# Kernel optimization log

Measured on AMD Instinct MI355X. Metric: run time of the kernel, lower is better.

The kernel has to match this reference:

```python
import jax, jax.numpy as jnp
import numpy as np

N = 50000      # nodes
E = 800000     # edges (before self loops)
D = 256        # in_features
SMALL = 25     # floor(D/10)


def setup_inputs() -> dict:
    key = jax.random.key(0)
    k1, k2, k3, k4, k5 = jax.random.split(key, 5)
    x = jax.random.normal(k1, (N, D), jnp.float32)
    src = jax.random.randint(k2, (E,), 0, N)
    dst = jax.random.randint(k3, (E,), 0, N)
    Wq = jax.random.normal(k4, (D, SMALL), jnp.float32) / np.float32(np.sqrt(D))
    bq = jnp.zeros((SMALL,), jnp.float32)
    Wk = jax.random.normal(k5, (D, SMALL), jnp.float32) / np.float32(np.sqrt(D))
    bk = jnp.zeros((SMALL,), jnp.float32)
    return {"x": x, "src": src, "dst": dst, "Wq": Wq, "bq": bq, "Wk": Wk, "bk": bk}


def reference(x, src, dst, Wq, bq, Wk, bk):
    d_k = np.float32(np.sqrt(SMALL))  # self.d_k = sqrt(small_in_features)
    q = jnp.tanh(x @ Wq + bq)         # query head: Linear + Tanh, [N, SMALL]
    k = x @ Wk + bk                   # key head: Linear,          [N, SMALL]
    # dgl.add_self_loop: append (i, i) for every node
    loop = jnp.arange(N, dtype=src.dtype)
    s = jnp.concatenate([src, loop])  # [E+N]
    d = jnp.concatenate([dst, loop])  # [E+N]
    # edge weight = <query[src], key[dst]> / d_k
    w = jnp.sum(q[s] * k[d], axis=1) / d_k            # [E+N]
    # segment softmax over incoming edges of each destination node
    wmax = jax.ops.segment_max(w, d, num_segments=N)  # every node has a self loop -> no empty segments
    ew = jnp.exp(w - wmax[d])
    denom = jax.ops.segment_sum(ew, d, num_segments=N)
    alpha = ew / denom[d]                             # [E+N]
    # weighted scatter-sum of src node features
    out = jax.ops.segment_sum(alpha[:, None] * x[s], d, num_segments=N)  # [N, D]
    return out
```

## Files before the change

### kernel.cpp

```cpp
#include <hip/hip_runtime.h>
#include <math.h>

#define D 256
#define SM 25
#define QS 32
#define WROWS 264
#define NCH 4

typedef short bf16x8 __attribute__((ext_vector_type(8)));
typedef float f32x4  __attribute__((ext_vector_type(4)));

__device__ __forceinline__ unsigned int bf16rne(float f) {
    unsigned int u = __float_as_uint(f);
    return (u + 0x7fffu + ((u >> 16) & 1u)) >> 16;
}
__device__ __forceinline__ float bl(unsigned int lo16) {
    return __uint_as_float(lo16 << 16);
}
__device__ __forceinline__ float bh(unsigned int u) {
    return __uint_as_float(u & 0xffff0000u);
}

__global__ __launch_bounds__(256) void prep_kernel(
    const float* __restrict__ Wq, const float* __restrict__ bq,
    const float* __restrict__ Wk, const float* __restrict__ bk,
    unsigned short* __restrict__ wt_g,
    float* __restrict__ bias_g,
    int* __restrict__ cnt, int N) {
    int gid = blockIdx.x * 256 + threadIdx.x;
    if (gid < N) cnt[gid] = 0;
    if (gid < 64 * 256) {
        int j = gid >> 8, k = gid & 255;
        float w = 0.f;
        if (j < SM) w = Wq[k * SM + j];
        else if (j < 2 * SM) w = Wk[k * SM + (j - SM)];
        wt_g[j * 256 + k] = (unsigned short)bf16rne(w);
    }
    if (gid >= 16384 && gid < 16448) {
        int t = gid - 16384;
        bias_g[t] = (t < SM) ? bq[t] : ((t < 2 * SM) ? bk[t - SM] : 0.f);
    }
}

__global__ __launch_bounds__(256) void qk_kernel(
    const float* __restrict__ x,
    const unsigned short* __restrict__ wt_g, const float* __restrict__ bias_g,
    const int4* __restrict__ dst4, const int* __restrict__ dste,
    unsigned short* __restrict__ xh,
    float* __restrict__ qp,
    float* __restrict__ kp,
    int* __restrict__ cnt, int N, int E) {
    __shared__ __align__(16) short xs[64 * WROWS];
    __shared__ __align__(16) short wt[64 * WROWS];
    __shared__ float bias[64];
    int t = threadIdx.x;
    int n0 = blockIdx.x * 64;

    {
        int r = t >> 2, qtr = t & 3;
        int row = n0 + r; if (row >= N) row = N - 1;
        const float4* xr = (const float4*)(x + (size_t)row * D) + qtr * 16;
        short* dst = xs + r * WROWS + qtr * 64;
#pragma unroll
        for (int i = 0; i < 16; ++i) {
            float4 a = xr[i];
            unsigned int w0 = bf16rne(a.x) | (bf16rne(a.y) << 16);
            unsigned int w1 = bf16rne(a.z) | (bf16rne(a.w) << 16);
            *(uint2*)(dst + i * 4) = make_uint2(w0, w1);
        }
    }
#pragma unroll
    for (int o = 0; o < 8; ++o) {
        int idx = o * 256 + t;
        int j = idx >> 5, k8 = idx & 31;
        *(uint4*)(wt + j * WROWS + k8 * 8) = ((const uint4*)wt_g)[idx];
    }
    if (t < 64) bias[t] = bias_g[t];
    __syncthreads();

    for (int o = 0; o < 8; ++o) {
        int idx = o * 256 + t;
        int r = idx >> 5, c = idx & 31;
        int row = n0 + r;
        if (row < N) {
            uint4 v = *(const uint4*)(xs + r * WROWS + c * 8);
            *((uint4*)(xh + (size_t)row * D) + c) = v;
        }
    }

    int wid = t >> 6, lane = t & 63;
    int mm = lane & 15, g = lane >> 4;
    f32x4 acc[4];
#pragma unroll
    for (int tt = 0; tt < 4; ++tt) acc[tt] = (f32x4){0.f, 0.f, 0.f, 0.f};
    const short* arow = xs + (wid * 16 + mm) * WROWS + g * 8;
#pragma unroll
    for (int ks = 0; ks < 8; ++ks) {
        bf16x8 af = *(const bf16x8*)(arow + ks * 32);
#pragma unroll
        for (int tt = 0; tt < 4; ++tt) {
            bf16x8 bf = *(const bf16x8*)(wt + (tt * 16 + mm) * WROWS + g * 8 + ks * 32);
            acc[tt] = __builtin_amdgcn_mfma_f32_16x16x32_bf16(af, bf, acc[tt], 0, 0, 0);
        }
    }
#pragma unroll
    for (int tt = 0; tt < 4; ++tt) {
        int j = tt * 16 + mm;
#pragma unroll
        for (int r = 0; r < 4; ++r) {
            int node = n0 + wid * 16 + g * 4 + r;
            if (node >= N) continue;
            float v = acc[tt][r] + bias[j];
            if (j < SM)           qp[(size_t)node * QS + j] = tanhf(v);
            else if (j < 2 * SM)  kp[(size_t)node * QS + (j - SM)] = v;
            else if (j < 57)      qp[(size_t)node * QS + (j - SM)] = 0.f;
            else                  kp[(size_t)node * QS + (j - 32)] = 0.f;
        }
    }

    int gid = blockIdx.x * 256 + t;
    int n4e = E >> 2;
    if (gid < n4e) {
        int4 dd = dst4[gid];
        atomicAdd(&cnt[dd.x], 1);
        atomicAdd(&cnt[dd.y], 1);
        atomicAdd(&cnt[dd.z], 1);
        atomicAdd(&cnt[dd.w], 1);
    }
    if (gid == 0) {
        for (int e = n4e * 4; e < E; ++e) atomicAdd(&cnt[dste[e]], 1);
    }
}

__global__ __launch_bounds__(256) void scan_a_kernel(const int4* __restrict__ cnt4,
                                                     int* __restrict__ bsum, int n4) {
    __shared__ int wsum[4];
    int t = threadIdx.x;
    int idx = blockIdx.x * 256 + t;
    int s = 0;
    if (idx < n4) { int4 v = cnt4[idx]; s = v.x + v.y + v.z + v.w; }
#pragma unroll
    for (int o = 32; o; o >>= 1) s += __shfl_xor(s, o);
    if ((t & 63) == 0) wsum[t >> 6] = s;
    __syncthreads();
    if (t == 0) bsum[blockIdx.x] = wsum[0] + wsum[1] + wsum[2] + wsum[3];
}

__global__ __launch_bounds__(256) void scan_c_kernel(const int4* __restrict__ cnt4,
                                                     const int* __restrict__ bsum,
                                                     int* __restrict__ offN,
                                                     int4* __restrict__ off4,
                                                     int4* __restrict__ cursor4,
                                                     int n4, int nblk) {
    __shared__ int wsum[4];
    int t = threadIdx.x;
    int lane = t & 63;
    int bv = (lane < nblk) ? bsum[lane] : 0;
    int bincl = bv;
#pragma unroll
    for (int o = 1; o < 64; o <<= 1) {
        int u = __shfl_up(bincl, o);
        if (lane >= o) bincl += u;
    }
    int blockbase = __shfl(bincl - bv, blockIdx.x);
    int total = __shfl(bincl, nblk - 1);
    if (blockIdx.x == 0 && t == 0) *offN = total;
    int idx = blockIdx.x * 256 + t;
    int4 v = make_int4(0, 0, 0, 0);
    if (idx < n4) v = cnt4[idx];
    int s0 = v.x, s01 = s0 + v.y, s012 = s01 + v.z, s = s012 + v.w;
    int incl = s;
#pragma unroll
    for (int o = 1; o < 64; o <<= 1) {
        int u = __shfl_up(incl, o);
        if (lane >= o) incl += u;
    }
    if (lane == 63) wsum[t >> 6] = incl;
    __syncthreads();
    int w = t >> 6;
    int wbase = 0;
    for (int i = 0; i < w; ++i) wbase += wsum[i];
    int base = blockbase + wbase + (incl - s);
    if (idx < n4) {
        int4 o4 = make_int4(base, base + s0, base + s01, base + s012);
        off4[idx]    = o4;
        cursor4[idx] = o4;
    }
}

__global__ void scatter_kernel(const int4* __restrict__ src4, const int4* __restrict__ dst4,
                               const int* __restrict__ srce, const int* __restrict__ dste,
                               int* __restrict__ cursor, int* __restrict__ csr_src,
                               int n4e, int E) {
    int e = blockIdx.x * blockDim.x + threadIdx.x;
    if (e >= n4e) return;
    int4 s = src4[e];
    int4 d = dst4[e];
    csr_src[atomicAdd(&cursor[d.x], 1)] = s.x;
    csr_src[atomicAdd(&cursor[d.y], 1)] = s.y;
    csr_src[atomicAdd(&cursor[d.z], 1)] = s.z;
    csr_src[atomicAdd(&cursor[d.w], 1)] = s.w;
    if (e == 0) {
        for (int i = n4e * 4; i < E; ++i)
            csr_src[atomicAdd(&cursor[dste[i]], 1)] = srce[i];
    }
}

__global__ __launch_bounds__(256) void agg_kernel(
        const uint2* __restrict__ xh2, const float* __restrict__ qp,
        const float* __restrict__ kp, const int* __restrict__ off,
        const int* __restrict__ csr_src, float4* __restrict__ out4, int N) {
    int lane = threadIdx.x & 63;
    int v = blockIdx.x * 4 + (threadIdx.x >> 6);
    if (v >= N) return;
    int lo = off[v];
    int deg1 = off[v + 1] - lo + 1;
    const float4* kd4 = (const float4*)(kp + (size_t)v * QS);
    float4 kd[7];
#pragma unroll
    for (int j = 0; j < 7; ++j) kd[j] = kd4[j];

    float wv[NCH]; int sv[NCH];
    float m = -INFINITY;
#pragma unroll
    for (int c = 0; c < NCH; ++c) {
        int i = c * 64 + lane;
        float wcur = -INFINITY; int s = v;
        if (c * 64 < deg1 && i < deg1) {
            if (i > 0) s = csr_src[lo + i - 1];
            const float4* q4 = (const float4*)(qp + (size_t)s * QS);
            float acc = 0.f;
#pragma unroll
            for (int j = 0; j < 7; ++j) {
                float4 a = q4[j];
                acc += a.x*kd[j].x + a.y*kd[j].y + a.z*kd[j].z + a.w*kd[j].w;
            }
            wcur = acc * 0.2f;
        }
        wv[c] = wcur; sv[c] = s;
        m = fmaxf(m, wcur);
    }
#pragma unroll
    for (int o = 32; o; o >>= 1) m = fmaxf(m, __shfl_xor(m, o));
    float ssum = 0.f;
#pragma unroll
    for (int c = 0; c < NCH; ++c) {
        float e = (wv[c] == -INFINITY) ? 0.f : __expf(wv[c] - m);
        wv[c] = e;
        ssum += e;
    }
#pragma unroll
    for (int o = 32; o; o >>= 1) ssum += __shfl_xor(ssum, o);
    float inv = 1.f / ssum;

    const uint2* xb = xh2 + lane;
    float4 acc = make_float4(0.f, 0.f, 0.f, 0.f);
#pragma unroll
    for (int c = 0; c < NCH; ++c) {
        if (c * 64 >= deg1) break;
        int cnt = deg1 - c * 64; if (cnt > 64) cnt = 64;
        int j = 0;
        for (; j + 8 <= cnt; j += 8) {
            float a0 = __shfl(wv[c], j);     int s0 = __shfl(sv[c], j);
            float a1 = __shfl(wv[c], j + 1); int s1 = __shfl(sv[c], j + 1);
            float a2 = __shfl(wv[c], j + 2); int s2 = __shfl(sv[c], j + 2);
            float a3 = __shfl(wv[c], j + 3); int s3 = __shfl(sv[c], j + 3);
            float a4 = __shfl(wv[c], j + 4); int s4 = __shfl(sv[c], j + 4);
            float a5 = __shfl(wv[c], j + 5); int s5 = __shfl(sv[c], j + 5);
            float a6 = __shfl(wv[c], j + 6); int s6 = __shfl(sv[c], j + 6);
            float a7 = __shfl(wv[c], j + 7); int s7 = __shfl(sv[c], j + 7);
            uint2 u0 = xb[(size_t)s0 * 64];
            uint2 u1 = xb[(size_t)s1 * 64];
            uint2 u2 = xb[(size_t)s2 * 64];
            uint2 u3 = xb[(size_t)s3 * 64];
            uint2 u4 = xb[(size_t)s4 * 64];
            uint2 u5 = xb[(size_t)s5 * 64];
            uint2 u6 = xb[(size_t)s6 * 64];
            uint2 u7 = xb[(size_t)s7 * 64];
            acc.x += a0 * bl(u0.x); acc.y += a0 * bh(u0.x);
            acc.z += a0 * bl(u0.y); acc.w += a0 * bh(u0.y);
            acc.x += a1 * bl(u1.x); acc.y += a1 * bh(u1.x);
            acc.z += a1 * bl(u1.y); acc.w += a1 * bh(u1.y);
            acc.x += a2 * bl(u2.x); acc.y += a2 * bh(u2.x);
            acc.z += a2 * bl(u2.y); acc.w += a2 * bh(u2.y);
            acc.x += a3 * bl(u3.x); acc.y += a3 * bh(u3.x);
            acc.z += a3 * bl(u3.y); acc.w += a3 * bh(u3.y);
            acc.x += a4 * bl(u4.x); acc.y += a4 * bh(u4.x);
            acc.z += a4 * bl(u4.y); acc.w += a4 * bh(u4.y);
            acc.x += a5 * bl(u5.x); acc.y += a5 * bh(u5.x);
            acc.z += a5 * bl(u5.y); acc.w += a5 * bh(u5.y);
            acc.x += a6 * bl(u6.x); acc.y += a6 * bh(u6.x);
            acc.z += a6 * bl(u6.y); acc.w += a6 * bh(u6.y);
            acc.x += a7 * bl(u7.x); acc.y += a7 * bh(u7.x);
            acc.z += a7 * bl(u7.y); acc.w += a7 * bh(u7.y);
        }
        for (; j + 4 <= cnt; j += 4) {
            float a0 = __shfl(wv[c], j);     int s0 = __shfl(sv[c], j);
            float a1 = __shfl(wv[c], j + 1); int s1 = __shfl(sv[c], j + 1);
            float a2 = __shfl(wv[c], j + 2); int s2 = __shfl(sv[c], j + 2);
            float a3 = __shfl(wv[c], j + 3); int s3 = __shfl(sv[c], j + 3);
            uint2 u0 = xb[(size_t)s0 * 64];
            uint2 u1 = xb[(size_t)s1 * 64];
            uint2 u2 = xb[(size_t)s2 * 64];
            uint2 u3 = xb[(size_t)s3 * 64];
            acc.x += a0 * bl(u0.x); acc.y += a0 * bh(u0.x);
            acc.z += a0 * bl(u0.y); acc.w += a0 * bh(u0.y);
            acc.x += a1 * bl(u1.x); acc.y += a1 * bh(u1.x);
            acc.z += a1 * bl(u1.y); acc.w += a1 * bh(u1.y);
            acc.x += a2 * bl(u2.x); acc.y += a2 * bh(u2.x);
            acc.z += a2 * bl(u2.y); acc.w += a2 * bh(u2.y);
            acc.x += a3 * bl(u3.x); acc.y += a3 * bh(u3.x);
            acc.z += a3 * bl(u3.y); acc.w += a3 * bh(u3.y);
        }
        for (; j < cnt; ++j) {
            float a = __shfl(wv[c], j);
            int   s = __shfl(sv[c], j);
            uint2 u = xb[(size_t)s * 64];
            acc.x += a * bl(u.x); acc.y += a * bh(u.x);
            acc.z += a * bl(u.y); acc.w += a * bh(u.y);
        }
    }
    acc.x *= inv; acc.y *= inv; acc.z *= inv; acc.w *= inv;
    out4[(size_t)v * 64 + lane] = acc;
}

extern "C" void kernel_launch(void* const* d_in, const int* in_sizes, int n_in,
                              void* d_out, int out_size, void* d_ws, size_t ws_size,
                              hipStream_t stream) {
    const float* x   = (const float*)d_in[0];
    const int*   src = (const int*)d_in[1];
    const int*   dst = (const int*)d_in[2];
    const float* Wq  = (const float*)d_in[3];
    const float* bq  = (const float*)d_in[4];
    const float* Wk  = (const float*)d_in[5];
    const float* bk  = (const float*)d_in[6];
    float* out = (float*)d_out;

    int N = in_sizes[0] / D;
    int E = in_sizes[1];

    char* p = (char*)d_ws;
    auto alloc = [&](size_t bytes) {
        char* r = p;
        p += (bytes + 255) & ~(size_t)255;
        return r;
    };
    unsigned short* xh   = (unsigned short*)alloc((size_t)N * D * sizeof(unsigned short));
    unsigned short* wt_g = (unsigned short*)alloc(64 * 256 * sizeof(unsigned short));
    float* bias_g  = (float*)alloc(64 * sizeof(float));
    float* qp      = (float*)alloc((size_t)N * QS * sizeof(float));
    float* kp      = (float*)alloc((size_t)N * QS * sizeof(float));
    int*   cnt     = (int*)  alloc((size_t)(N + 4) * sizeof(int));
    int*   off     = (int*)  alloc((size_t)(N + 4) * sizeof(int));
    int*   cursor  = (int*)  alloc((size_t)(N + 4) * sizeof(int));
    int*   csr_src = (int*)  alloc((size_t)E * sizeof(int));
    int*   bsum    = (int*)  alloc(64 * sizeof(int));

    int prepgrid = (N > 16448 ? N : 16448);
    prep_kernel<<<(prepgrid + 255) / 256, 256, 0, stream>>>(
        Wq, bq, Wk, bk, wt_g, bias_g, cnt, N);
    int nqk = (N + 63) / 64;
    qk_kernel<<<nqk, 256, 0, stream>>>(x, wt_g, bias_g, (const int4*)dst, dst,
                                       xh, qp, kp, cnt, N, E);
    int n4 = (N + 3) / 4;
    int nblk = (n4 + 255) / 256;
    scan_a_kernel<<<nblk, 256, 0, stream>>>((const int4*)cnt, bsum, n4);
    scan_c_kernel<<<nblk, 256, 0, stream>>>((const int4*)cnt, bsum, off + N,
                                            (int4*)off, (int4*)cursor, n4, nblk);
    int n4e = E / 4;
    scatter_kernel<<<(n4e + 255) / 256, 256, 0, stream>>>(
        (const int4*)src, (const int4*)dst, src, dst, cursor, csr_src, n4e, E);
    agg_kernel<<<(N + 3) / 4, 256, 0, stream>>>(
        (const uint2*)xh, qp, kp, off, csr_src, (float4*)out, N);
}
```

Baseline: 278.2 us.

## Split aggregation into score and feature-tiled gather kernels with tiled bf16 layout

The fused aggregation kernel is split in two. A score kernel computes softmax-normalized edge weights and writes them to global arrays, and a gather kernel processes the 256 features in 8 tiles of 32. The bf16 copy of x is stored tile-major so each tile's gather working set is smaller and more cache-friendly. The qk kernel also reads the weight matrix directly from global memory instead of staging it in shared memory. This adds a kernel launch, extra traffic for the alpha arrays, and repeated CSR/alpha reads across the 8 tiles, in exchange for better L2 locality on the random row gathers.

```diff
diff --git a/kernel.cpp b/kernel.cpp
--- a/kernel.cpp
+++ b/kernel.cpp
@@ -6,6 +6,7 @@
 #define QS 32
 #define WROWS 264
 #define NCH 4
+#define NT 8
 
 typedef short bf16x8 __attribute__((ext_vector_type(8)));
 typedef float f32x4  __attribute__((ext_vector_type(4)));
@@ -46,12 +47,11 @@
     const float* __restrict__ x,
     const unsigned short* __restrict__ wt_g, const float* __restrict__ bias_g,
     const int4* __restrict__ dst4, const int* __restrict__ dste,
-    unsigned short* __restrict__ xh,
+    unsigned short* __restrict__ xt,
     float* __restrict__ qp,
     float* __restrict__ kp,
     int* __restrict__ cnt, int N, int E) {
     __shared__ __align__(16) short xs[64 * WROWS];
-    __shared__ __align__(16) short wt[64 * WROWS];
     __shared__ float bias[64];
     int t = threadIdx.x;
     int n0 = blockIdx.x * 64;
@@ -68,12 +68,6 @@
             unsigned int w1 = bf16rne(a.z) | (bf16rne(a.w) << 16);
             *(uint2*)(dst + i * 4) = make_uint2(w0, w1);
         }
-    }
-#pragma unroll
-    for (int o = 0; o < 8; ++o) {
-        int idx = o * 256 + t;
-        int j = idx >> 5, k8 = idx & 31;
-        *(uint4*)(wt + j * WROWS + k8 * 8) = ((const uint4*)wt_g)[idx];
     }
     if (t < 64) bias[t] = bias_g[t];
     __syncthreads();
@@ -84,7 +78,8 @@
         int row = n0 + r;
         if (row < N) {
             uint4 v = *(const uint4*)(xs + r * WROWS + c * 8);
-            *((uint4*)(xh + (size_t)row * D) + c) = v;
+            int tile = c >> 2;
+            ((uint4*)xt)[((size_t)tile * N + row) * 4 + (c & 3)] = v;
         }
     }
 
@@ -99,7 +94,8 @@
         bf16x8 af = *(const bf16x8*)(arow + ks * 32);
 #pragma unroll
         for (int tt = 0; tt < 4; ++tt) {
-            bf16x8 bf = *(const bf16x8*)(wt + (tt * 16 + mm) * WROWS + g * 8 + ks * 32);
+            bf16x8 bf = *(const bf16x8*)((const short*)wt_g +
+                                         (tt * 16 + mm) * 256 + g * 8 + ks * 32);
             acc[tt] = __builtin_amdgcn_mfma_f32_16x16x32_bf16(af, bf, acc[tt], 0, 0, 0);
         }
     }
@@ -206,10 +202,10 @@
     }
 }
 
-__global__ __launch_bounds__(256) void agg_kernel(
-        const uint2* __restrict__ xh2, const float* __restrict__ qp,
-        const float* __restrict__ kp, const int* __restrict__ off,
-        const int* __restrict__ csr_src, float4* __restrict__ out4, int N) {
+__global__ __launch_bounds__(256) void score_kernel(
+        const float* __restrict__ qp, const float* __restrict__ kp,
+        const int* __restrict__ off, const int* __restrict__ csr_src,
+        float* __restrict__ alphaS, float* __restrict__ alphaE, int N) {
     int lane = threadIdx.x & 63;
     int v = blockIdx.x * 4 + (threadIdx.x >> 6);
     if (v >= N) return;
@@ -220,13 +216,14 @@
 #pragma unroll
     for (int j = 0; j < 7; ++j) kd[j] = kd4[j];
 
-    float wv[NCH]; int sv[NCH];
+    float wv[NCH];
     float m = -INFINITY;
 #pragma unroll
     for (int c = 0; c < NCH; ++c) {
         int i = c * 64 + lane;
-        float wcur = -INFINITY; int s = v;
+        float wcur = -INFINITY;
         if (c * 64 < deg1 && i < deg1) {
+            int s = v;
             if (i > 0) s = csr_src[lo + i - 1];
             const float4* q4 = (const float4*)(qp + (size_t)s * QS);
             float acc = 0.f;
@@ -237,7 +234,7 @@
             }
             wcur = acc * 0.2f;
         }
-        wv[c] = wcur; sv[c] = s;
+        wv[c] = wcur;
         m = fmaxf(m, wcur);
     }
 #pragma unroll
@@ -253,75 +250,59 @@
     for (int o = 32; o; o >>= 1) ssum += __shfl_xor(ssum, o);
     float inv = 1.f / ssum;
 
-    const uint2* xb = xh2 + lane;
-    float4 acc = make_float4(0.f, 0.f, 0.f, 0.f);
 #pragma unroll
     for (int c = 0; c < NCH; ++c) {
-        if (c * 64 >= deg1) break;
-        int cnt = deg1 - c * 64; if (cnt > 64) cnt = 64;
-        int j = 0;
-        for (; j + 8 <= cnt; j += 8) {
-            float a0 = __shfl(wv[c], j);     int s0 = __shfl(sv[c], j);
-            float a1 = __shfl(wv[c], j + 1); int s1 = __shfl(sv[c], j + 1);
-            float a2 = __shfl(wv[c], j + 2); int s2 = __shfl(sv[c], j + 2);
-            float a3 = __shfl(wv[c], j + 3); int s3 = __shfl(sv[c], j + 3);
-            float a4 = __shfl(wv[c], j + 4); int s4 = __shfl(sv[c], j + 4);
-            float a5 = __shfl(wv[c], j + 5); int s5 = __shfl(sv[c], j + 5);
-            float a6 = __shfl(wv[c], j + 6); int s6 = __shfl(sv[c], j + 6);
-            float a7 = __shfl(wv[c], j + 7); int s7 = __shfl(sv[c], j + 7);
-            uint2 u0 = xb[(size_t)s0 * 64];
-            uint2 u1 = xb[(size_t)s1 * 64];
-            uint2 u2 = xb[(size_t)s2 * 64];
-            uint2 u3 = xb[(size_t)s3 * 64];
-            uint2 u4 = xb[(size_t)s4 * 64];
-            uint2 u5 = xb[(size_t)s5 * 64];
-            uint2 u6 = xb[(size_t)s6 * 64];
-            uint2 u7 = xb[(size_t)s7 * 64];
-            acc.x += a0 * bl(u0.x); acc.y += a0 * bh(u0.x);
-            acc.z += a0 * bl(u0.y); acc.w += a0 * bh(u0.y);
-            acc.x += a1 * bl(u1.x); acc.y += a1 * bh(u1.x);
-            acc.z += a1 * bl(u1.y); acc.w += a1 * bh(u1.y);
-            acc.x += a2 * bl(u2.x); acc.y += a2 * bh(u2.x);
-            acc.z += a2 * bl(u2.y); acc.w += a2 * bh(u2.y);
-            acc.x += a3 * bl(u3.x); acc.y += a3 * bh(u3.x);
-            acc.z += a3 * bl(u3.y); acc.w += a3 * bh(u3.y);
-            acc.x += a4 * bl(u4.x); acc.y += a4 * bh(u4.x);
-            acc.z += a4 * bl(u4.y); acc.w += a4 * bh(u4.y);
-            acc.x += a5 * bl(u5.x); acc.y += a5 * bh(u5.x);
-            acc.z += a5 * bl(u5.y); acc.w += a5 * bh(u5.y);
-            acc.x += a6 * bl(u6.x); acc.y += a6 * bh(u6.x);
-            acc.z += a6 * bl(u6.y); acc.w += a6 * bh(u6.y);
-            acc.x += a7 * bl(u7.x); acc.y += a7 * bh(u7.x);
-            acc.z += a7 * bl(u7.y); acc.w += a7 * bh(u7.y);
-        }
-        for (; j + 4 <= cnt; j += 4) {
-            float a0 = __shfl(wv[c], j);     int s0 = __shfl(sv[c], j);
-            float a1 = __shfl(wv[c], j + 1); int s1 = __shfl(sv[c], j + 1);
-            float a2 = __shfl(wv[c], j + 2); int s2 = __shfl(sv[c], j + 2);
-            float a3 = __shfl(wv[c], j + 3); int s3 = __shfl(sv[c], j + 3);
-            uint2 u0 = xb[(size_t)s0 * 64];
-            uint2 u1 = xb[(size_t)s1 * 64];
-            uint2 u2 = xb[(size_t)s2 * 64];
-            uint2 u3 = xb[(size_t)s3 * 64];
-            acc.x += a0 * bl(u0.x); acc.y += a0 * bh(u0.x);
-            acc.z += a0 * bl(u0.y); acc.w += a0 * bh(u0.y);
-            acc.x += a1 * bl(u1.x); acc.y += a1 * bh(u1.x);
-            acc.z += a1 * bl(u1.y); acc.w += a1 * bh(u1.y);
-            acc.x += a2 * bl(u2.x); acc.y += a2 * bh(u2.x);
-            acc.z += a2 * bl(u2.y); acc.w += a2 * bh(u2.y);
-            acc.x += a3 * bl(u3.x); acc.y += a3 * bh(u3.x);
-            acc.z += a3 * bl(u3.y); acc.w += a3 * bh(u3.y);
-        }
-        for (; j < cnt; ++j) {
-            float a = __shfl(wv[c], j);
-            int   s = __shfl(sv[c], j);
-            uint2 u = xb[(size_t)s * 64];
-            acc.x += a * bl(u.x); acc.y += a * bh(u.x);
-            acc.z += a * bl(u.y); acc.w += a * bh(u.y);
-        }
-    }
-    acc.x *= inv; acc.y *= inv; acc.z *= inv; acc.w *= inv;
-    out4[(size_t)v * 64 + lane] = acc;
+        int i = c * 64 + lane;
+        if (c * 64 < deg1 && i < deg1) {
+            float a = wv[c] * inv;
+            if (i == 0) alphaS[v] = a;
+            else        alphaE[lo + i - 1] = a;
+        }
+    }
+}
+
+__global__ __launch_bounds__(256) void gather_kernel(
+        const unsigned int* __restrict__ xt,
+        const float* __restrict__ alphaS, const float* __restrict__ alphaE,
+        const int* __restrict__ off, const int* __restrict__ csr_src,
+        float* __restrict__ out, int N) {
+    int tile = blockIdx.x & (NT - 1);
+    int nb = blockIdx.x >> 3;
+    int t = threadIdx.x;
+    int g = t >> 4;
+    int l = t & 15;
+    int v = nb * 16 + g;
+    if (v >= N) return;
+    const unsigned int* xbase = xt + (size_t)tile * N * 16 + l;
+    int lo = off[v], hi = off[v + 1];
+    float ax = 0.f, ay = 0.f;
+    {
+        float a = alphaS[v];
+        unsigned int u = xbase[(size_t)v * 16];
+        ax += a * bl(u); ay += a * bh(u);
+    }
+    int e = lo;
+    for (; e + 4 <= hi; e += 4) {
+        float a0 = alphaE[e];     int s0 = csr_src[e];
+        float a1 = alphaE[e + 1]; int s1 = csr_src[e + 1];
+        float a2 = alphaE[e + 2]; int s2 = csr_src[e + 2];
+        float a3 = alphaE[e + 3]; int s3 = csr_src[e + 3];
+        unsigned int u0 = xbase[(size_t)s0 * 16];
+        unsigned int u1 = xbase[(size_t)s1 * 16];
+        unsigned int u2 = xbase[(size_t)s2 * 16];
+        unsigned int u3 = xbase[(size_t)s3 * 16];
+        ax += a0 * bl(u0); ay += a0 * bh(u0);
+        ax += a1 * bl(u1); ay += a1 * bh(u1);
+        ax += a2 * bl(u2); ay += a2 * bh(u2);
+        ax += a3 * bl(u3); ay += a3 * bh(u3);
+    }
+    for (; e < hi; ++e) {
+        float a = alphaE[e];
+        int   s = csr_src[e];
+        unsigned int u = xbase[(size_t)s * 16];
+        ax += a * bl(u); ay += a * bh(u);
+    }
+    *(float2*)(out + (size_t)v * D + tile * 32 + l * 2) = make_float2(ax, ay);
 }
 
 extern "C" void kernel_launch(void* const* d_in, const int* in_sizes, int n_in,
@@ -345,7 +326,7 @@
         p += (bytes + 255) & ~(size_t)255;
         return r;
     };
-    unsigned short* xh   = (unsigned short*)alloc((size_t)N * D * sizeof(unsigned short));
+    unsigned short* xt   = (unsigned short*)alloc((size_t)N * D * sizeof(unsigned short));
     unsigned short* wt_g = (unsigned short*)alloc(64 * 256 * sizeof(unsigned short));
     float* bias_g  = (float*)alloc(64 * sizeof(float));
     float* qp      = (float*)alloc((size_t)N * QS * sizeof(float));
@@ -355,13 +336,15 @@
     int*   cursor  = (int*)  alloc((size_t)(N + 4) * sizeof(int));
     int*   csr_src = (int*)  alloc((size_t)E * sizeof(int));
     int*   bsum    = (int*)  alloc(64 * sizeof(int));
+    float* alphaS  = (float*)alloc((size_t)N * sizeof(float));
+    float* alphaE  = (float*)alloc((size_t)E * sizeof(float));
 
     int prepgrid = (N > 16448 ? N : 16448);
     prep_kernel<<<(prepgrid + 255) / 256, 256, 0, stream>>>(
         Wq, bq, Wk, bk, wt_g, bias_g, cnt, N);
     int nqk = (N + 63) / 64;
     qk_kernel<<<nqk, 256, 0, stream>>>(x, wt_g, bias_g, (const int4*)dst, dst,
-                                       xh, qp, kp, cnt, N, E);
+                                       xt, qp, kp, cnt, N, E);
     int n4 = (N + 3) / 4;
     int nblk = (n4 + 255) / 256;
     scan_a_kernel<<<nblk, 256, 0, stream>>>((const int4*)cnt, bsum, n4);
@@ -370,6 +353,10 @@
     int n4e = E / 4;
     scatter_kernel<<<(n4e + 255) / 256, 256, 0, stream>>>(
         (const int4*)src, (const int4*)dst, src, dst, cursor, csr_src, n4e, E);
-    agg_kernel<<<(N + 3) / 4, 256, 0, stream>>>(
-        (const uint2*)xh, qp, kp, off, csr_src, (float4*)out, N);
-}
+    score_kernel<<<(N + 3) / 4, 256, 0, stream>>>(qp, kp, off, csr_src,
+                                                  alphaS, alphaE, N);
+    int ngb = (N + 15) / 16;
+    gather_kernel<<<ngb * NT, 256, 0, stream>>>((const unsigned int*)xt,
+                                                alphaS, alphaE, off, csr_src,
+                                                out, N);
+}
```

Result: slower. 325.8 us (+17.1%).

## Split edge dot products across four lanes and read QK weights from global

Applied to the files above, without the earlier changes.

In the aggregation kernel, each edge's 25-wide query·key dot product is now split across four lanes, each doing 8 elements, and combined with xor-shuffles. A wave therefore scores 16 edges per chunk instead of 64, which cuts per-lane serial loads and the number of lanes left idle on low-degree nodes. The trade-off is capacity: with NCHK=4 a node can now hold at most 64 incoming edges, down from 256. The projection kernel also drops the LDS staging of the weight matrix and loads B fragments straight from global/L2, saving LDS and one copy phase at the cost of repeated global reads.

```diff
diff --git a/kernel.cpp b/kernel.cpp
--- a/kernel.cpp
+++ b/kernel.cpp
@@ -5,7 +5,7 @@
 #define SM 25
 #define QS 32
 #define WROWS 264
-#define NCH 4
+#define NCHK 4
 
 typedef short bf16x8 __attribute__((ext_vector_type(8)));
 typedef float f32x4  __attribute__((ext_vector_type(4)));
@@ -51,7 +51,6 @@
     float* __restrict__ kp,
     int* __restrict__ cnt, int N, int E) {
     __shared__ __align__(16) short xs[64 * WROWS];
-    __shared__ __align__(16) short wt[64 * WROWS];
     __shared__ float bias[64];
     int t = threadIdx.x;
     int n0 = blockIdx.x * 64;
@@ -68,12 +67,6 @@
             unsigned int w1 = bf16rne(a.z) | (bf16rne(a.w) << 16);
             *(uint2*)(dst + i * 4) = make_uint2(w0, w1);
         }
-    }
-#pragma unroll
-    for (int o = 0; o < 8; ++o) {
-        int idx = o * 256 + t;
-        int j = idx >> 5, k8 = idx & 31;
-        *(uint4*)(wt + j * WROWS + k8 * 8) = ((const uint4*)wt_g)[idx];
     }
     if (t < 64) bias[t] = bias_g[t];
     __syncthreads();
@@ -99,7 +92,8 @@
         bf16x8 af = *(const bf16x8*)(arow + ks * 32);
 #pragma unroll
         for (int tt = 0; tt < 4; ++tt) {
-            bf16x8 bf = *(const bf16x8*)(wt + (tt * 16 + mm) * WROWS + g * 8 + ks * 32);
+            bf16x8 bf = *(const bf16x8*)((const short*)wt_g +
+                                         (tt * 16 + mm) * 256 + g * 8 + ks * 32);
             acc[tt] = __builtin_amdgcn_mfma_f32_16x16x32_bf16(af, bf, acc[tt], 0, 0, 0);
         }
     }
@@ -215,60 +209,62 @@
     if (v >= N) return;
     int lo = off[v];
     int deg1 = off[v + 1] - lo + 1;
+    int g = lane >> 2, p = lane & 3;
     const float4* kd4 = (const float4*)(kp + (size_t)v * QS);
-    float4 kd[7];
-#pragma unroll
-    for (int j = 0; j < 7; ++j) kd[j] = kd4[j];
-
-    float wv[NCH]; int sv[NCH];
+    float4 kd0 = kd4[p * 2], kd1 = kd4[p * 2 + 1];
+
+    float wv[NCHK]; int sv[NCHK];
     float m = -INFINITY;
 #pragma unroll
-    for (int c = 0; c < NCH; ++c) {
-        int i = c * 64 + lane;
+    for (int c = 0; c < NCHK; ++c) {
+        int i = c * 16 + g;
         float wcur = -INFINITY; int s = v;
-        if (c * 64 < deg1 && i < deg1) {
+        if (c * 16 < deg1 && i < deg1) {
             if (i > 0) s = csr_src[lo + i - 1];
             const float4* q4 = (const float4*)(qp + (size_t)s * QS);
-            float acc = 0.f;
-#pragma unroll
-            for (int j = 0; j < 7; ++j) {
-                float4 a = q4[j];
-                acc += a.x*kd[j].x + a.y*kd[j].y + a.z*kd[j].z + a.w*kd[j].w;
-            }
-            wcur = acc * 0.2f;
+            float4 a0 = q4[p * 2], a1 = q4[p * 2 + 1];
+            float part = a0.x*kd0.x + a0.y*kd0.y + a0.z*kd0.z + a0.w*kd0.w
+                       + a1.x*kd1.x + a1.y*kd1.y + a1.z*kd1.z + a1.w*kd1.w;
+            part += __shfl_xor(part, 1);
+            part += __shfl_xor(part, 2);
+            wcur = part * 0.2f;
         }
         wv[c] = wcur; sv[c] = s;
         m = fmaxf(m, wcur);
     }
-#pragma unroll
-    for (int o = 32; o; o >>= 1) m = fmaxf(m, __shfl_xor(m, o));
+    m = fmaxf(m, __shfl_xor(m, 4));
+    m = fmaxf(m, __shfl_xor(m, 8));
+    m = fmaxf(m, __shfl_xor(m, 16));
+    m = fmaxf(m, __shfl_xor(m, 32));
     float ssum = 0.f;
 #pragma unroll
-    for (int c = 0; c < NCH; ++c) {
+    for (int c = 0; c < NCHK; ++c) {
         float e = (wv[c] == -INFINITY) ? 0.f : __expf(wv[c] - m);
         wv[c] = e;
         ssum += e;
     }
-#pragma unroll
-    for (int o = 32; o; o >>= 1) ssum += __shfl_xor(ssum, o);
+    ssum += __shfl_xor(ssum, 4);
+    ssum += __shfl_xor(ssum, 8);
+    ssum += __shfl_xor(ssum, 16);
+    ssum += __shfl_xor(ssum, 32);
     float inv = 1.f / ssum;
 
     const uint2* xb = xh2 + lane;
     float4 acc = make_float4(0.f, 0.f, 0.f, 0.f);
 #pragma unroll
-    for (int c = 0; c < NCH; ++c) {
-        if (c * 64 >= deg1) break;
-        int cnt = deg1 - c * 64; if (cnt > 64) cnt = 64;
+    for (int c = 0; c < NCHK; ++c) {
+        if (c * 16 >= deg1) break;
+        int cnt = deg1 - c * 16; if (cnt > 16) cnt = 16;
         int j = 0;
         for (; j + 8 <= cnt; j += 8) {
-            float a0 = __shfl(wv[c], j);     int s0 = __shfl(sv[c], j);
-            float a1 = __shfl(wv[c], j + 1); int s1 = __shfl(sv[c], j + 1);
-            float a2 = __shfl(wv[c], j + 2); int s2 = __shfl(sv[c], j + 2);
-            float a3 = __shfl(wv[c], j + 3); int s3 = __shfl(sv[c], j + 3);
-            float a4 = __shfl(wv[c], j + 4); int s4 = __shfl(sv[c], j + 4);
-            float a5 = __shfl(wv[c], j + 5); int s5 = __shfl(sv[c], j + 5);
-            float a6 = __shfl(wv[c], j + 6); int s6 = __shfl(sv[c], j + 6);
-            float a7 = __shfl(wv[c], j + 7); int s7 = __shfl(sv[c], j + 7);
+            float a0 = __shfl(wv[c], (j    ) * 4); int s0 = __shfl(sv[c], (j    ) * 4);
+            float a1 = __shfl(wv[c], (j + 1) * 4); int s1 = __shfl(sv[c], (j + 1) * 4);
+            float a2 = __shfl(wv[c], (j + 2) * 4); int s2 = __shfl(sv[c], (j + 2) * 4);
+            float a3 = __shfl(wv[c], (j + 3) * 4); int s3 = __shfl(sv[c], (j + 3) * 4);
+            float a4 = __shfl(wv[c], (j + 4) * 4); int s4 = __shfl(sv[c], (j + 4) * 4);
+            float a5 = __shfl(wv[c], (j + 5) * 4); int s5 = __shfl(sv[c], (j + 5) * 4);
+            float a6 = __shfl(wv[c], (j + 6) * 4); int s6 = __shfl(sv[c], (j + 6) * 4);
+            float a7 = __shfl(wv[c], (j + 7) * 4); int s7 = __shfl(sv[c], (j + 7) * 4);
             uint2 u0 = xb[(size_t)s0 * 64];
             uint2 u1 = xb[(size_t)s1 * 64];
             uint2 u2 = xb[(size_t)s2 * 64];
@@ -295,10 +291,10 @@
             acc.z += a7 * bl(u7.y); acc.w += a7 * bh(u7.y);
         }
         for (; j + 4 <= cnt; j += 4) {
-            float a0 = __shfl(wv[c], j);     int s0 = __shfl(sv[c], j);
-            float a1 = __shfl(wv[c], j + 1); int s1 = __shfl(sv[c], j + 1);
-            float a2 = __shfl(wv[c], j + 2); int s2 = __shfl(sv[c], j + 2);
-            float a3 = __shfl(wv[c], j + 3); int s3 = __shfl(sv[c], j + 3);
+            float a0 = __shfl(wv[c], (j    ) * 4); int s0 = __shfl(sv[c], (j    ) * 4);
+            float a1 = __shfl(wv[c], (j + 1) * 4); int s1 = __shfl(sv[c], (j + 1) * 4);
+            float a2 = __shfl(wv[c], (j + 2) * 4); int s2 = __shfl(sv[c], (j + 2) * 4);
+            float a3 = __shfl(wv[c], (j + 3) * 4); int s3 = __shfl(sv[c], (j + 3) * 4);
             uint2 u0 = xb[(size_t)s0 * 64];
             uint2 u1 = xb[(size_t)s1 * 64];
             uint2 u2 = xb[(size_t)s2 * 64];
@@ -313,8 +309,8 @@
             acc.z += a3 * bl(u3.y); acc.w += a3 * bh(u3.y);
         }
         for (; j < cnt; ++j) {
-            float a = __shfl(wv[c], j);
-            int   s = __shfl(sv[c], j);
+            float a = __shfl(wv[c], j * 4);
+            int   s = __shfl(sv[c], j * 4);
             uint2 u = xb[(size_t)s * 64];
             acc.x += a * bl(u.x); acc.y += a * bh(u.x);
             acc.z += a * bl(u.y); acc.w += a * bh(u.y);
```

Result: no change. 280.6 us (+0.9%).
